# Optimization experiments

Hardware: AMD Instinct MI355X
Metric: run time of the kernel (lower is better)

## Reference

```python
import jax, jax.numpy as jnp
import numpy as np

POOL, D_MODEL, D_FF, M_DIM = 512, 1024, 4096, 64
B, S, K = 2, 2048, 8


def setup_inputs() -> dict:
    key = jax.random.key(0)
    ks = jax.random.split(key, 8)
    x = jax.random.normal(ks[0], (B, S, D_MODEL), dtype=jnp.float32)
    selected_indices = jax.random.randint(ks[1], (B, S, K), 0, POOL, dtype=jnp.int32)
    pattern_weights = jax.random.normal(ks[2], (B, S, K), dtype=jnp.float32)
    base_patterns = 0.02 * jax.random.normal(ks[3], (POOL, D_FF), dtype=jnp.float32)
    # nn.Linear(d_model, pool_size*mod_dim): weight [P*M, d_model], xavier-uniform
    lim_cm = float(np.sqrt(6.0 / (D_MODEL + POOL * M_DIM)))
    cm_w = jax.random.uniform(ks[4], (POOL * M_DIM, D_MODEL), jnp.float32, -lim_cm, lim_cm)
    cm_b = jnp.zeros((POOL * M_DIM,), jnp.float32)
    adj_proj = 0.01 * jax.random.normal(ks[5], (M_DIM, D_FF), dtype=jnp.float32)
    lim_w2 = float(np.sqrt(6.0 / (D_FF + D_MODEL)))
    w2_w = jax.random.uniform(ks[6], (D_MODEL, D_FF), jnp.float32, -lim_w2, lim_w2)
    w2_b = jnp.zeros((D_MODEL,), jnp.float32)
    return {"x": x, "selected_indices": selected_indices, "pattern_weights": pattern_weights,
            "base_patterns": base_patterns, "cm_w": cm_w, "cm_b": cm_b,
            "adj_proj": adj_proj, "w2_w": w2_w, "w2_b": w2_b}


def reference(x, selected_indices, pattern_weights, base_patterns, cm_w, cm_b, adj_proj, w2_w, w2_b):
    b, s, k = selected_indices.shape
    # gather base firing patterns for selected neurons: [b,s,k,d_ff]
    bp = base_patterns[selected_indices]
    # dense context modulation then gather (matches original module): [b,s,P,M]
    mod = (jnp.einsum('bsd,nd->bsn', x, cm_w) + cm_b).reshape(b, s, POOL, M_DIM)
    sel_mod = jnp.take_along_axis(mod, selected_indices[..., None], axis=2)  # [b,s,k,M]
    adjustments = jnp.einsum('bskm,mf->bskf', sel_mod, adj_proj)
    adjusted = bp + adjustments  # [b,s,k,d_ff]
    w = jax.nn.softmax(pattern_weights, axis=-1)
    combined = jnp.einsum('bsk,bskf->bsf', w, adjusted)  # [b,s,d_ff]
    activated = jax.nn.gelu(combined, approximate=False)  # torch default gelu = exact erf
    return jnp.einsum('bsf,df->bsd', activated, w2_w) + w2_b
```

## Files before the change

kernel.cpp:

```cpp
#include <hip/hip_runtime.h>
#include <math.h>

#define T_    4096
#define K_    8
#define POOL_ 512
#define DM_   1024
#define DFF_  4096
#define MD_   64
#define KC_   576

typedef __bf16 bf16x8 __attribute__((ext_vector_type(8)));
typedef __bf16 bf16x4 __attribute__((ext_vector_type(4)));
typedef float  f32x4  __attribute__((ext_vector_type(4)));

typedef __attribute__((address_space(1))) const void g_void;
typedef __attribute__((address_space(3))) void s_void;

__device__ __forceinline__ void async_ld16(const void* g, void* s) {
    __builtin_amdgcn_global_load_lds((g_void*)g, (s_void*)s, 16, 0, 0);
}
__device__ __forceinline__ float gelu_exact(float g) {
    return 0.5f * g * (1.f + erff(g * 0.70710678118654752f));
}

__global__ __launch_bounds__(256) void k_hist(const int* __restrict__ sel,
                                              int* __restrict__ counts) {
    int i = blockIdx.x * 256 + threadIdx.x;
    if (i < T_ * K_) atomicAdd(&counts[sel[i]], 1);
}

__global__ __launch_bounds__(512) void k_scan(const int* __restrict__ counts,
                                              int* __restrict__ offsets,
                                              int* __restrict__ cursor) {
    __shared__ int s[512];
    const int t = threadIdx.x;
    const int c = counts[t];
    s[t] = c;
    __syncthreads();
    for (int d = 1; d < 512; d <<= 1) {
        int v = (t >= d) ? s[t - d] : 0;
        __syncthreads();
        s[t] += v;
        __syncthreads();
    }
    offsets[t] = s[t] - c;
    cursor[t]  = s[t] - c;
    if (t == 511) offsets[512] = s[511];
}

__global__ __launch_bounds__(256) void k_scatter(const int* __restrict__ sel,
                                                 int* __restrict__ cursor,
                                                 int* __restrict__ bucket) {
    int i = blockIdx.x * 256 + threadIdx.x;
    if (i < T_ * K_) {
        int p = sel[i];
        int pos = atomicAdd(&cursor[p], 1);
        bucket[pos] = i;
    }
}

__global__ __launch_bounds__(256) void k_selmod(
    const float* __restrict__ x, const float* __restrict__ cm_w,
    const float* __restrict__ cm_b, const int* __restrict__ bucket,
    const int* __restrict__ offsets, float* __restrict__ Y)
{
    const int p   = blockIdx.x;
    const int tid = threadIdx.x;
    __shared__ int list[1024];
    __shared__ __align__(16) __bf16 Xl[64][136];
    __shared__ __align__(16) __bf16 Wl[64][136];

    const int off = offsets[p];
    const int n   = min(offsets[p + 1] - off, 1024);
    for (int i = tid; i < n; i += 256) list[i] = bucket[off + i];
    __syncthreads();
    if (n == 0) return;

    const int wave = tid >> 6, lane = tid & 63, quad = lane >> 4, l15 = lane & 15;
    const int srow = tid & 63;
    const int c0   = (tid >> 6) * 32;

    const float* wrow = cm_w + (long)(p * 64 + srow) * DM_;

    for (int base = 0; base < n; base += 64) {
        f32x4 acc[4] = {};
        int li = base + srow; if (li >= n) li = n - 1;
        const float* xrow = x + (long)(list[li] >> 3) * DM_;

        for (int kc = 0; kc < DM_; kc += 128) {
            const float4* xs = (const float4*)(xrow + kc + c0);
            const float4* ws = (const float4*)(wrow + kc + c0);
            #pragma unroll
            for (int u = 0; u < 8; ++u) {
                float4 xv = xs[u], wv = ws[u];
                bf16x4 xb, wb;
                xb[0]=(__bf16)xv.x; xb[1]=(__bf16)xv.y; xb[2]=(__bf16)xv.z; xb[3]=(__bf16)xv.w;
                wb[0]=(__bf16)wv.x; wb[1]=(__bf16)wv.y; wb[2]=(__bf16)wv.z; wb[3]=(__bf16)wv.w;
                *(bf16x4*)&Xl[srow][c0 + u * 4] = xb;
                *(bf16x4*)&Wl[srow][c0 + u * 4] = wb;
            }
            __syncthreads();
            #pragma unroll
            for (int ks = 0; ks < 4; ++ks) {
                const int ko = ks * 32 + quad * 8;
                bf16x8 bfr = *(const bf16x8*)&Wl[wave * 16 + l15][ko];
                #pragma unroll
                for (int i = 0; i < 4; ++i) {
                    bf16x8 afr = *(const bf16x8*)&Xl[i * 16 + l15][ko];
                    acc[i] = __builtin_amdgcn_mfma_f32_16x16x32_bf16(afr, bfr, acc[i], 0, 0, 0);
                }
            }
            __syncthreads();
        }
        const int   mcol = wave * 16 + l15;
        const float bias = cm_b[p * 64 + mcol];
        #pragma unroll
        for (int i = 0; i < 4; ++i) {
            #pragma unroll
            for (int r = 0; r < 4; ++r) {
                int prow = base + i * 16 + quad * 4 + r;
                if (prow < n)
                    Y[(long)list[prow] * MD_ + mcol] = acc[i][r] + bias;
            }
        }
    }
}

__global__ __launch_bounds__(256) void k_wdense(
    const float* __restrict__ Y, const int* __restrict__ sel,
    const float* __restrict__ pw, __bf16* __restrict__ Wd)
{
    const int tid = threadIdx.x;
    const int tt = tid >> 6, m = tid & 63;
    const int t = blockIdx.x * 4 + tt;
    __shared__ float w_s[4][8];
    __shared__ int   sidx[4][8];
    __shared__ __align__(16) __bf16 row[4][KC_];

    if (m < 8) {
        w_s[tt][m]  = pw[t * 8 + m];
        sidx[tt][m] = sel[t * 8 + m];
    }
    __syncthreads();
    if (m == 0) {
        float mx = w_s[tt][0];
        #pragma unroll
        for (int k = 1; k < 8; ++k) mx = fmaxf(mx, w_s[tt][k]);
        float sum = 0.f;
        #pragma unroll
        for (int k = 0; k < 8; ++k) { float e = expf(w_s[tt][k] - mx); w_s[tt][k] = e; sum += e; }
        float inv = 1.f / sum;
        #pragma unroll
        for (int k = 0; k < 8; ++k) w_s[tt][k] *= inv;
    }
    __syncthreads();
    *(uint4*)&row[tt][m * 8] = make_uint4(0, 0, 0, 0);
    float a = 0.f;
    #pragma unroll
    for (int k = 0; k < 8; ++k) a += w_s[tt][k] * Y[((long)t * 8 + k) * MD_ + m];
    row[tt][512 + m] = (__bf16)a;
    __syncthreads();
    if (m == 0) {
        #pragma unroll
        for (int k = 0; k < 8; ++k) {
            int c = sidx[tt][k];
            row[tt][c] = (__bf16)((float)row[tt][c] + w_s[tt][k]);
        }
    }
    __syncthreads();
    const uint4* src = (const uint4*)&row[0][0];
    uint4* dst = (uint4*)(Wd + (long)blockIdx.x * 4 * KC_);
    for (int e = tid; e < 4 * KC_ * 2 / 16; e += 256) dst[e] = src[e];
}

__global__ __launch_bounds__(256) void k_buildP(
    const float* __restrict__ bp, const float* __restrict__ adj,
    __bf16* __restrict__ P)
{
    __shared__ __bf16 tile[64][72];
    const int tid = threadIdx.x;
    const int bx = blockIdx.x, f0 = blockIdx.y * 64;
    const float* src = (bx < 8) ? (bp + (long)bx * 64 * DFF_) : adj;
    for (int e = tid; e < 4096; e += 256) {
        int f = e & 63, c = e >> 6;
        tile[c][f] = (__bf16)src[(long)c * DFF_ + f0 + f];
    }
    __syncthreads();
    const int c0 = bx * 64;
    for (int e = tid; e < 4096; e += 256) {
        int c = e & 63, f = e >> 6;
        P[(long)(f0 + f) * KC_ + c0 + c] = tile[c][f];
    }
}

__global__ __launch_bounds__(256) void k_cvt(const float* __restrict__ src,
                                             __bf16* __restrict__ dst, int n16) {
    int i = blockIdx.x * 256 + threadIdx.x;
    if (i >= n16) return;
    const float4* s = (const float4*)src + (long)i * 4;
    float4 a = s[0], b = s[1], c = s[2], d = s[3];
    bf16x8 o0, o1;
    o0[0]=(__bf16)a.x; o0[1]=(__bf16)a.y; o0[2]=(__bf16)a.z; o0[3]=(__bf16)a.w;
    o0[4]=(__bf16)b.x; o0[5]=(__bf16)b.y; o0[6]=(__bf16)b.z; o0[7]=(__bf16)b.w;
    o1[0]=(__bf16)c.x; o1[1]=(__bf16)c.y; o1[2]=(__bf16)c.z; o1[3]=(__bf16)c.w;
    o1[4]=(__bf16)d.x; o1[5]=(__bf16)d.y; o1[6]=(__bf16)d.z; o1[7]=(__bf16)d.w;
    bf16x8* dp = (bf16x8*)dst + (long)i * 2;
    dp[0] = o0; dp[1] = o1;
}

__global__ __launch_bounds__(256) void k_actgemm(
    const __bf16* __restrict__ A, const __bf16* __restrict__ Bw,
    __bf16* __restrict__ act)
{
    __shared__ __align__(16) __bf16 sA[128 * 32];
    __shared__ __align__(16) __bf16 sB[128 * 32];
    const int tid  = threadIdx.x;
    const int tm   = blockIdx.y * 128, tn = blockIdx.x * 128;
    const int wave = tid >> 6, lane = tid & 63, quad = lane >> 4, l15 = lane & 15;
    const int wm   = (wave >> 1) * 64, wn = (wave & 1) * 64;

    f32x4 acc[4][4] = {};

    const int e    = tid * 8;
    const int srow = e >> 5;
    const int scol = e & 31;
    const __bf16* agp0 = A  + ((long)(tm + srow)      * KC_ + scol);
    const __bf16* agp1 = A  + ((long)(tm + 64 + srow) * KC_ + scol);
    const __bf16* bgp0 = Bw + ((long)(tn + srow)      * KC_ + scol);
    const __bf16* bgp1 = Bw + ((long)(tn + 64 + srow) * KC_ + scol);
    void* sa0 = (void*)(sA + e);
    void* sa1 = (void*)(sA + 2048 + e);
    void* sb0 = (void*)(sB + e);
    void* sb1 = (void*)(sB + 2048 + e);

    for (int kk = 0; kk < KC_; kk += 32) {
        async_ld16(agp0 + kk, sa0);
        async_ld16(agp1 + kk, sa1);
        async_ld16(bgp0 + kk, sb0);
        async_ld16(bgp1 + kk, sb1);
        __syncthreads();
        bf16x8 af[4], bf[4];
        #pragma unroll
        for (int i = 0; i < 4; ++i)
            af[i] = *(const bf16x8*)(sA + (wm + i * 16 + l15) * 32 + quad * 8);
        #pragma unroll
        for (int j = 0; j < 4; ++j)
            bf[j] = *(const bf16x8*)(sB + (wn + j * 16 + l15) * 32 + quad * 8);
        #pragma unroll
        for (int i = 0; i < 4; ++i)
            #pragma unroll
            for (int j = 0; j < 4; ++j)
                acc[i][j] = __builtin_amdgcn_mfma_f32_16x16x32_bf16(af[i], bf[j], acc[i][j], 0, 0, 0);
        __syncthreads();
    }

    #pragma unroll
    for (int j = 0; j < 4; ++j) {
        const int col = tn + wn + j * 16 + l15;
        #pragma unroll
        for (int i = 0; i < 4; ++i) {
            const int row = tm + wm + i * 16 + quad * 4;
            #pragma unroll
            for (int r = 0; r < 4; ++r)
                act[(long)(row + r) * DFF_ + col] = (__bf16)gelu_exact(acc[i][j][r]);
        }
    }
}

__global__ __launch_bounds__(256) void k_outgemm(
    const __bf16* __restrict__ A, const __bf16* __restrict__ Bw,
    const float* __restrict__ bias, float* __restrict__ out)
{
    __shared__ __align__(16) __bf16 sA[128 * 32];
    __shared__ __align__(16) __bf16 sB[128 * 32];
    const int tid  = threadIdx.x;
    const int tm   = blockIdx.y * 128, tn = blockIdx.x * 128;
    const int wave = tid >> 6, lane = tid & 63, quad = lane >> 4, l15 = lane & 15;
    const int wm   = (wave >> 1) * 64, wn = (wave & 1) * 64;

    f32x4 acc[4][4] = {};

    const int e    = tid * 8;
    const int srow = e >> 5;
    const int scol = e & 31;
    const __bf16* agp0 = A  + ((long)(tm + srow)      * DFF_ + scol);
    const __bf16* agp1 = A  + ((long)(tm + 64 + srow) * DFF_ + scol);
    const __bf16* bgp0 = Bw + ((long)(tn + srow)      * DFF_ + scol);
    const __bf16* bgp1 = Bw + ((long)(tn + 64 + srow) * DFF_ + scol);
    void* sa0 = (void*)(sA + e);
    void* sa1 = (void*)(sA + 2048 + e);
    void* sb0 = (void*)(sB + e);
    void* sb1 = (void*)(sB + 2048 + e);

    for (int kk = 0; kk < DFF_; kk += 32) {
        async_ld16(agp0 + kk, sa0);
        async_ld16(agp1 + kk, sa1);
        async_ld16(bgp0 + kk, sb0);
        async_ld16(bgp1 + kk, sb1);
        __syncthreads();
        bf16x8 af[4], bf[4];
        #pragma unroll
        for (int i = 0; i < 4; ++i)
            af[i] = *(const bf16x8*)(sA + (wm + i * 16 + l15) * 32 + quad * 8);
        #pragma unroll
        for (int j = 0; j < 4; ++j)
            bf[j] = *(const bf16x8*)(sB + (wn + j * 16 + l15) * 32 + quad * 8);
        #pragma unroll
        for (int i = 0; i < 4; ++i)
            #pragma unroll
            for (int j = 0; j < 4; ++j)
                acc[i][j] = __builtin_amdgcn_mfma_f32_16x16x32_bf16(af[i], bf[j], acc[i][j], 0, 0, 0);
        __syncthreads();
    }

    #pragma unroll
    for (int j = 0; j < 4; ++j) {
        const int col = tn + wn + j * 16 + l15;
        const float bj = bias[col];
        #pragma unroll
        for (int i = 0; i < 4; ++i) {
            const int row = tm + wm + i * 16 + quad * 4;
            #pragma unroll
            for (int r = 0; r < 4; ++r)
                out[(long)(row + r) * 1024 + col] = acc[i][j][r] + bj;
        }
    }
}

extern "C" void kernel_launch(void* const* d_in, const int* in_sizes, int n_in,
                              void* d_out, int out_size, void* d_ws, size_t ws_size,
                              hipStream_t stream) {
    const float* x    = (const float*)d_in[0];
    const int*   sel  = (const int*)  d_in[1];
    const float* pw   = (const float*)d_in[2];
    const float* bp   = (const float*)d_in[3];
    const float* cm_w = (const float*)d_in[4];
    const float* cm_b = (const float*)d_in[5];
    const float* adj  = (const float*)d_in[6];
    const float* w2   = (const float*)d_in[7];
    const float* w2b  = (const float*)d_in[8];
    float* out = (float*)d_out;

    char* ws = (char*)d_ws;
    __bf16* act  = (__bf16*)ws;
    __bf16* P    = (__bf16*)(ws + (size_t)32 * 1024 * 1024);
    __bf16* w2bf = (__bf16*)(ws + (size_t)37 * 1024 * 1024);
    char*  bins  = ws + (size_t)45 * 1024 * 1024;
    int* bucket  = (int*)bins;
    int* counts  = (int*)(bins + 131072);
    int* cursor  = (int*)(bins + 133120);
    int* offsets = (int*)(bins + 135168);

    float*  Y  = (float*)d_out;
    __bf16* Wd = (__bf16*)((char*)d_out + (size_t)8 * 1024 * 1024);

    hipMemsetAsync(counts, 0, 4096, stream);
    k_hist   <<<128, 256, 0, stream>>>(sel, counts);
    k_scan   <<<1,   512, 0, stream>>>(counts, offsets, cursor);
    k_scatter<<<128, 256, 0, stream>>>(sel, cursor, bucket);
    k_selmod <<<POOL_, 256, 0, stream>>>(x, cm_w, cm_b, bucket, offsets, Y);
    k_wdense <<<T_ / 4, 256, 0, stream>>>(Y, sel, pw, Wd);
    k_buildP <<<dim3(9, 64), 256, 0, stream>>>(bp, adj, P);
    k_cvt    <<<1024, 256, 0, stream>>>(w2, w2bf, DM_ * DFF_ / 16);
    k_actgemm<<<dim3(DFF_ / 128, T_ / 128), 256, 0, stream>>>(Wd, P, act);
    k_outgemm<<<dim3(DM_ / 128, T_ / 128), 256, 0, stream>>>(act, w2bf, w2b, out);
}
```

Measured before the change: 432.2 us.

## Split-K the selected-modulation GEMM and deepen the output GEMM K-tile

The per-pool modulation GEMM is split four ways along d_model across a second grid dimension. Each slice writes partial results to workspace, and the weighting kernel sums the partials and adds the bias. This is meant to raise occupancy and parallelism in the previously 512-block selmod kernel. The output GEMM now stages 128-wide K chunks per barrier instead of 32, which cuts synchronisations but uses more LDS and adds extra partial-sum traffic.

```diff
diff --git a/kernel.cpp b/kernel.cpp
--- a/kernel.cpp
+++ b/kernel.cpp
@@ -8,6 +8,7 @@
 #define DFF_  4096
 #define MD_   64
 #define KC_   576
+#define NSPLIT 4
 
 typedef __bf16 bf16x8 __attribute__((ext_vector_type(8)));
 typedef __bf16 bf16x4 __attribute__((ext_vector_type(4)));
@@ -59,39 +60,39 @@
     }
 }
 
-__global__ __launch_bounds__(256) void k_selmod(
+__global__ __launch_bounds__(256, 8) void k_selmod(
     const float* __restrict__ x, const float* __restrict__ cm_w,
-    const float* __restrict__ cm_b, const int* __restrict__ bucket,
-    const int* __restrict__ offsets, float* __restrict__ Y)
-{
-    const int p   = blockIdx.x;
-    const int tid = threadIdx.x;
-    __shared__ int list[1024];
-    __shared__ __align__(16) __bf16 Xl[64][136];
-    __shared__ __align__(16) __bf16 Wl[64][136];
+    const int* __restrict__ bucket, const int* __restrict__ offsets,
+    float* __restrict__ Yp)
+{
+    const int p     = blockIdx.x;
+    const int slice = blockIdx.y;
+    const int tid   = threadIdx.x;
+    __shared__ __align__(16) __bf16 Xl[64][72];
+    __shared__ __align__(16) __bf16 Wl[64][72];
 
     const int off = offsets[p];
     const int n   = min(offsets[p + 1] - off, 1024);
-    for (int i = tid; i < n; i += 256) list[i] = bucket[off + i];
-    __syncthreads();
     if (n == 0) return;
 
     const int wave = tid >> 6, lane = tid & 63, quad = lane >> 4, l15 = lane & 15;
     const int srow = tid & 63;
-    const int c0   = (tid >> 6) * 32;
-
-    const float* wrow = cm_w + (long)(p * 64 + srow) * DM_;
+    const int c0   = (tid >> 6) * 16;
+    const int k0   = slice * (DM_ / NSPLIT);
+
+    const float* wrow = cm_w + (long)(p * 64 + srow) * DM_ + k0;
+    float* Yo = Yp + (long)slice * ((long)T_ * K_ * MD_);
 
     for (int base = 0; base < n; base += 64) {
         f32x4 acc[4] = {};
         int li = base + srow; if (li >= n) li = n - 1;
-        const float* xrow = x + (long)(list[li] >> 3) * DM_;
-
-        for (int kc = 0; kc < DM_; kc += 128) {
+        const float* xrow = x + (long)(bucket[off + li] >> 3) * DM_ + k0;
+
+        for (int kc = 0; kc < DM_ / NSPLIT; kc += 64) {
             const float4* xs = (const float4*)(xrow + kc + c0);
             const float4* ws = (const float4*)(wrow + kc + c0);
             #pragma unroll
-            for (int u = 0; u < 8; ++u) {
+            for (int u = 0; u < 4; ++u) {
                 float4 xv = xs[u], wv = ws[u];
                 bf16x4 xb, wb;
                 xb[0]=(__bf16)xv.x; xb[1]=(__bf16)xv.y; xb[2]=(__bf16)xv.z; xb[3]=(__bf16)xv.w;
@@ -101,7 +102,7 @@
             }
             __syncthreads();
             #pragma unroll
-            for (int ks = 0; ks < 4; ++ks) {
+            for (int ks = 0; ks < 2; ++ks) {
                 const int ko = ks * 32 + quad * 8;
                 bf16x8 bfr = *(const bf16x8*)&Wl[wave * 16 + l15][ko];
                 #pragma unroll
@@ -112,23 +113,23 @@
             }
             __syncthreads();
         }
-        const int   mcol = wave * 16 + l15;
-        const float bias = cm_b[p * 64 + mcol];
+        const int mcol = wave * 16 + l15;
         #pragma unroll
         for (int i = 0; i < 4; ++i) {
             #pragma unroll
             for (int r = 0; r < 4; ++r) {
                 int prow = base + i * 16 + quad * 4 + r;
                 if (prow < n)
-                    Y[(long)list[prow] * MD_ + mcol] = acc[i][r] + bias;
+                    Yo[(long)bucket[off + prow] * MD_ + mcol] = acc[i][r];
             }
         }
     }
 }
 
 __global__ __launch_bounds__(256) void k_wdense(
-    const float* __restrict__ Y, const int* __restrict__ sel,
-    const float* __restrict__ pw, __bf16* __restrict__ Wd)
+    const float* __restrict__ Yp, const int* __restrict__ sel,
+    const float* __restrict__ pw, const float* __restrict__ cm_b,
+    __bf16* __restrict__ Wd)
 {
     const int tid = threadIdx.x;
     const int tt = tid >> 6, m = tid & 63;
@@ -155,10 +156,19 @@
     }
     __syncthreads();
     *(uint4*)&row[tt][m * 8] = make_uint4(0, 0, 0, 0);
-    float a = 0.f;
-    #pragma unroll
-    for (int k = 0; k < 8; ++k) a += w_s[tt][k] * Y[((long)t * 8 + k) * MD_ + m];
-    row[tt][512 + m] = (__bf16)a;
+    {
+        const long YN = (long)T_ * K_ * MD_;
+        float a = 0.f;
+        #pragma unroll
+        for (int k = 0; k < 8; ++k) {
+            const long base = ((long)t * 8 + k) * MD_ + m;
+            float y = cm_b[sidx[tt][k] * 64 + m];
+            #pragma unroll
+            for (int s = 0; s < NSPLIT; ++s) y += Yp[s * YN + base];
+            a += w_s[tt][k] * y;
+        }
+        row[tt][512 + m] = (__bf16)a;
+    }
     __syncthreads();
     if (m == 0) {
         #pragma unroll
@@ -271,8 +281,8 @@
     const __bf16* __restrict__ A, const __bf16* __restrict__ Bw,
     const float* __restrict__ bias, float* __restrict__ out)
 {
-    __shared__ __align__(16) __bf16 sA[128 * 32];
-    __shared__ __align__(16) __bf16 sB[128 * 32];
+    __shared__ __align__(16) __bf16 sA[128 * 128];
+    __shared__ __align__(16) __bf16 sB[128 * 128];
     const int tid  = threadIdx.x;
     const int tm   = blockIdx.y * 128, tn = blockIdx.x * 128;
     const int wave = tid >> 6, lane = tid & 63, quad = lane >> 4, l15 = lane & 15;
@@ -280,36 +290,37 @@
 
     f32x4 acc[4][4] = {};
 
-    const int e    = tid * 8;
-    const int srow = e >> 5;
-    const int scol = e & 31;
-    const __bf16* agp0 = A  + ((long)(tm + srow)      * DFF_ + scol);
-    const __bf16* agp1 = A  + ((long)(tm + 64 + srow) * DFF_ + scol);
-    const __bf16* bgp0 = Bw + ((long)(tn + srow)      * DFF_ + scol);
-    const __bf16* bgp1 = Bw + ((long)(tn + 64 + srow) * DFF_ + scol);
-    void* sa0 = (void*)(sA + e);
-    void* sa1 = (void*)(sA + 2048 + e);
-    void* sb0 = (void*)(sB + e);
-    void* sb1 = (void*)(sB + 2048 + e);
-
-    for (int kk = 0; kk < DFF_; kk += 32) {
-        async_ld16(agp0 + kk, sa0);
-        async_ld16(agp1 + kk, sa1);
-        async_ld16(bgp0 + kk, sb0);
-        async_ld16(bgp1 + kk, sb1);
-        __syncthreads();
-        bf16x8 af[4], bf[4];
-        #pragma unroll
-        for (int i = 0; i < 4; ++i)
-            af[i] = *(const bf16x8*)(sA + (wm + i * 16 + l15) * 32 + quad * 8);
-        #pragma unroll
-        for (int j = 0; j < 4; ++j)
-            bf[j] = *(const bf16x8*)(sB + (wn + j * 16 + l15) * 32 + quad * 8);
-        #pragma unroll
-        for (int i = 0; i < 4; ++i)
+    const int e  = tid * 8;
+    const int r0 = e >> 5;
+    const int cc = e & 31;
+
+    for (int kk = 0; kk < DFF_; kk += 128) {
+        #pragma unroll
+        for (int s = 0; s < 4; ++s) {
+            #pragma unroll
+            for (int q = 0; q < 2; ++q) {
+                async_ld16(A  + (long)(tm + q * 64 + r0) * DFF_ + kk + s * 32 + cc,
+                           (void*)(sA + s * 4096 + q * 2048 + e));
+                async_ld16(Bw + (long)(tn + q * 64 + r0) * DFF_ + kk + s * 32 + cc,
+                           (void*)(sB + s * 4096 + q * 2048 + e));
+            }
+        }
+        __syncthreads();
+        #pragma unroll
+        for (int s = 0; s < 4; ++s) {
+            bf16x8 af[4], bf[4];
+            #pragma unroll
+            for (int i = 0; i < 4; ++i)
+                af[i] = *(const bf16x8*)(sA + s * 4096 + (wm + i * 16 + l15) * 32 + quad * 8);
             #pragma unroll
             for (int j = 0; j < 4; ++j)
-                acc[i][j] = __builtin_amdgcn_mfma_f32_16x16x32_bf16(af[i], bf[j], acc[i][j], 0, 0, 0);
+                bf[j] = *(const bf16x8*)(sB + s * 4096 + (wn + j * 16 + l15) * 32 + quad * 8);
+            #pragma unroll
+            for (int i = 0; i < 4; ++i)
+                #pragma unroll
+                for (int j = 0; j < 4; ++j)
+                    acc[i][j] = __builtin_amdgcn_mfma_f32_16x16x32_bf16(af[i], bf[j], acc[i][j], 0, 0, 0);
+        }
         __syncthreads();
     }
 
@@ -342,6 +353,7 @@
     float* out = (float*)d_out;
 
     char* ws = (char*)d_ws;
+    float*  Yp   = (float*)ws;
     __bf16* act  = (__bf16*)ws;
     __bf16* P    = (__bf16*)(ws + (size_t)32 * 1024 * 1024);
     __bf16* w2bf = (__bf16*)(ws + (size_t)37 * 1024 * 1024);
@@ -351,15 +363,14 @@
     int* cursor  = (int*)(bins + 133120);
     int* offsets = (int*)(bins + 135168);
 
-    float*  Y  = (float*)d_out;
-    __bf16* Wd = (__bf16*)((char*)d_out + (size_t)8 * 1024 * 1024);
+    __bf16* Wd = (__bf16*)d_out;
 
     hipMemsetAsync(counts, 0, 4096, stream);
     k_hist   <<<128, 256, 0, stream>>>(sel, counts);
     k_scan   <<<1,   512, 0, stream>>>(counts, offsets, cursor);
     k_scatter<<<128, 256, 0, stream>>>(sel, cursor, bucket);
-    k_selmod <<<POOL_, 256, 0, stream>>>(x, cm_w, cm_b, bucket, offsets, Y);
-    k_wdense <<<T_ / 4, 256, 0, stream>>>(Y, sel, pw, Wd);
+    k_selmod <<<dim3(POOL_, NSPLIT), 256, 0, stream>>>(x, cm_w, bucket, offsets, Yp);
+    k_wdense <<<T_ / 4, 256, 0, stream>>>(Yp, sel, pw, cm_b, Wd);
     k_buildP <<<dim3(9, 64), 256, 0, stream>>>(bp, adj, P);
     k_cvt    <<<1024, 256, 0, stream>>>(w2, w2bf, DM_ * DFF_ / 16);
     k_actgemm<<<dim3(DFF_ / 128, T_ / 128), 256, 0, stream>>>(Wd, P, act);
```

New measurement: 441.2 us. 1.02x slower.
